# Kernel tuning notes

Hardware: AMD Instinct MI355X
Metric: run time of the kernel (lower is better)

## Reference

```python
import jax, jax.numpy as jnp
import numpy as np

N = 100000   # total nodes
E = 500000   # directed edges
G = 100      # graphs in batch (1000 nodes each)
D = 146      # in/hidden/out dim
C = 10       # classes
BN_EPS = 1e-5


def setup_inputs():
    key = jax.random.key(0)
    ks = jax.random.split(key, 20)
    nodes_feat = jax.random.normal(ks[0], (N, D), jnp.float32)
    src = jax.random.randint(ks[1], (E,), 0, N, dtype=jnp.int32)
    dst = jax.random.randint(ks[2], (E,), 0, N, dtype=jnp.int32)
    graph_ids = (jnp.arange(N, dtype=jnp.int32) // (N // G)).astype(jnp.int32)
    snorm = jnp.full((N,), 1.0 / np.sqrt(N // G), jnp.float32)
    s = 0.05
    W_emb = jax.random.normal(ks[3], (D, D), jnp.float32) * s
    b_emb = jnp.zeros((D,), jnp.float32)
    Ws = jax.random.normal(ks[4], (4, D, D), jnp.float32) * s
    bs = jnp.zeros((4, D), jnp.float32)
    gammas = jnp.ones((4, D), jnp.float32)
    betas = jnp.zeros((4, D), jnp.float32)
    W1 = jax.random.normal(ks[5], (D, D // 2), jnp.float32) * s
    b1 = jnp.zeros((D // 2,), jnp.float32)
    W2 = jax.random.normal(ks[6], (D // 2, D // 4), jnp.float32) * s
    b2 = jnp.zeros((D // 4,), jnp.float32)
    W3 = jax.random.normal(ks[7], (D // 4, C), jnp.float32) * s
    b3 = jnp.zeros((C,), jnp.float32)
    return dict(nodes_feat=nodes_feat, snorm=snorm, W_emb=W_emb, b_emb=b_emb,
                Ws=Ws, bs=bs, gammas=gammas, betas=betas,
                W1=W1, b1=b1, W2=W2, b2=b2, W3=W3, b3=b3,
                src=src, dst=dst, graph_ids=graph_ids)


def _gcn_layer(h, W, b, gamma, beta, src, dst, norm_out, norm_in, snorm):
    h_in = h
    # GraphConv norm='both': D_out^{-1/2} on source, sum-aggregate, D_in^{-1/2} on dest
    m = (h * norm_out[:, None])[src]                     # [E, D] gather
    agg = jax.ops.segment_sum(m, dst, num_segments=N)    # [N, D] scatter-add
    h = agg * norm_in[:, None] @ W + b                   # linear
    h = h * snorm[:, None]                               # graph norm
    mu = jnp.mean(h, axis=0)
    var = jnp.var(h, axis=0)
    h = (h - mu) * jax.lax.rsqrt(var + BN_EPS) * gamma + beta  # batch norm
    h = jax.nn.relu(h)
    return h_in + h                                      # residual


def reference(nodes_feat, snorm, W_emb, b_emb, Ws, bs, gammas, betas,
              W1, b1, W2, b2, W3, b3, src, dst, graph_ids):
    ones_e = jnp.ones((E,), jnp.float32)
    deg_out = jnp.clip(jax.ops.segment_sum(ones_e, src, num_segments=N), 1.0)
    deg_in = jnp.clip(jax.ops.segment_sum(ones_e, dst, num_segments=N), 1.0)
    norm_out = jax.lax.rsqrt(deg_out)
    norm_in = jax.lax.rsqrt(deg_in)

    h = nodes_feat @ W_emb + b_emb                       # embedding_h
    for i in range(4):
        h = _gcn_layer(h, Ws[i], bs[i], gammas[i], betas[i],
                       src, dst, norm_out, norm_in, snorm)

    # mean_nodes per graph
    cnt = jax.ops.segment_sum(jnp.ones((N,), jnp.float32), graph_ids, num_segments=G)
    hg = jax.ops.segment_sum(h, graph_ids, num_segments=G) / cnt[:, None]

    # MLPReadout: 146 -> 73 -> 36 -> 10
    x = jax.nn.relu(hg @ W1 + b1)
    x = jax.nn.relu(x @ W2 + b2)
    return x @ W3 + b3
```

## Files before the change

kernel.cpp:

```cpp
#include <hip/hip_runtime.h>

#define N_NODES 100000
#define N_EDGES 500000
#define N_GRAPHS 100
#define DIM 146
#define APAD 160
#define HPAD 160
#define TPW 160
#define BN_EPS 1e-5f
#define GS_PART 8
#define GS_STRIDE 147
#define ST_PART 4

typedef __bf16 bf16x8 __attribute__((ext_vector_type(8)));
typedef float floatx4 __attribute__((ext_vector_type(4)));
typedef unsigned short ushort_t;
typedef unsigned int uint_t;

__device__ inline ushort_t f2bf(float x) {
  uint_t u = __float_as_uint(x);
  uint_t r = (u + 0x7fffu + ((u >> 16) & 1u)) >> 16;
  return (ushort_t)r;
}
__device__ inline float bf2f(ushort_t b) { return __uint_as_float((uint_t)b << 16); }
__device__ inline uint_t pack2bf(float a, float b) {
  return (uint_t)f2bf(a) | ((uint_t)f2bf(b) << 16);
}
__device__ inline float bflo(uint_t u) { return __uint_as_float(u << 16); }
__device__ inline float bfhi(uint_t u) { return __uint_as_float(u & 0xffff0000u); }

__device__ inline void async_cp16(const ushort_t* g, ushort_t* l) {
  __builtin_amdgcn_global_load_lds((const __attribute__((address_space(1))) void*)g,
                                   (__attribute__((address_space(3))) void*)l, 16, 0, 0);
}

__global__ void hist_kernel(const int* __restrict__ src, const int* __restrict__ dst,
                            int* __restrict__ deg_out, int* __restrict__ deg_in) {
  int e = blockIdx.x * 256 + threadIdx.x;
  if (e < N_EDGES) {
    atomicAdd(&deg_out[src[e]], 1);
    atomicAdd(&deg_in[dst[e]], 1);
  }
}

__global__ void norm_kernel(const int* __restrict__ deg_out, const int* __restrict__ deg_in,
                            float* __restrict__ norm_out, float* __restrict__ norm_in) {
  int v = blockIdx.x * 256 + threadIdx.x;
  if (v < N_NODES) {
    norm_out[v] = rsqrtf((float)max(deg_out[v], 1));
    norm_in[v]  = rsqrtf((float)max(deg_in[v], 1));
  }
}

__global__ void scan1_kernel(const int* __restrict__ deg_in, int* __restrict__ bsums) {
  __shared__ int sred[256];
  int t0 = blockIdx.x * 1024 + threadIdx.x * 4;
  int s = 0;
#pragma unroll
  for (int i = 0; i < 4; i++) { int v = t0 + i; s += (v < N_NODES) ? deg_in[v] : 0; }
  sred[threadIdx.x] = s; __syncthreads();
  for (int off = 128; off > 0; off >>= 1) {
    if (threadIdx.x < off) sred[threadIdx.x] += sred[threadIdx.x + off];
    __syncthreads();
  }
  if (threadIdx.x == 0) bsums[blockIdx.x] = sred[0];
}

__global__ void scan2_kernel(const int* __restrict__ bsums, int* __restrict__ bofs,
                             int* __restrict__ row_ptr, int nb) {
  if (threadIdx.x == 0 && blockIdx.x == 0) {
    int run = 0;
    for (int i = 0; i < nb; i++) { bofs[i] = run; run += bsums[i]; }
    row_ptr[N_NODES] = run;
  }
}

__global__ void scan3_kernel(const int* __restrict__ deg_in, const int* __restrict__ bofs,
                             int* __restrict__ row_ptr) {
  __shared__ int ssc[256];
  int t0 = blockIdx.x * 1024 + threadIdx.x * 4;
  int v4[4]; int s = 0;
#pragma unroll
  for (int i = 0; i < 4; i++) { int v = t0 + i; v4[i] = (v < N_NODES) ? deg_in[v] : 0; s += v4[i]; }
  ssc[threadIdx.x] = s; __syncthreads();
  for (int off = 1; off < 256; off <<= 1) {
    int t = (threadIdx.x >= off) ? ssc[threadIdx.x - off] : 0;
    __syncthreads();
    ssc[threadIdx.x] += t;
    __syncthreads();
  }
  int ex = ssc[threadIdx.x] - s + bofs[blockIdx.x];
#pragma unroll
  for (int i = 0; i < 4; i++) {
    int v = t0 + i;
    if (v < N_NODES) { row_ptr[v] = ex; ex += v4[i]; }
  }
}

__global__ void csr_fill_kernel(const int* __restrict__ src, const int* __restrict__ dst,
                                const int* __restrict__ row_ptr, int* __restrict__ fill,
                                int* __restrict__ csr) {
  int e = blockIdx.x * 256 + threadIdx.x;
  if (e < N_EDGES) {
    int d = dst[e];
    int slot = atomicAdd(&fill[d], 1);
    csr[row_ptr[d] + slot] = src[e];
  }
}

__global__ void wtrans_kernel(const float* __restrict__ W_emb, const float* __restrict__ Ws,
                              ushort_t* __restrict__ Wb, ushort_t* __restrict__ Wh) {
  int idx = blockIdx.x * 256 + threadIdx.x;
  if (idx >= 5 * 5 * 10 * 64 * 8) return;
  int j = idx & 7;
  int t = idx >> 3;
  int lane = t & 63; t >>= 6;
  int nt = t % 10; t /= 10;
  int kc = t % 5;
  int m = t / 5;
  const float* W = (m == 0) ? W_emb : Ws + (size_t)(m - 1) * DIM * DIM;
  int k = kc * 32 + (lane >> 4) * 8 + j;
  int n = nt * 16 + (lane & 15);
  float w = (k < DIM && n < DIM) ? W[k * DIM + n] : 0.f;
  ushort_t hi = f2bf(w);
  float lo = w - bf2f(hi);
  size_t base = (size_t)((((m * 5 + kc) * 10 + nt) * 2) * 64 + lane) * 8 + j;
  Wb[base] = hi;
  Wb[base + 512] = f2bf(lo);
  Wh[(size_t)(((m * 5 + kc) * 10 + nt) * 64 + lane) * 8 + j] = hi;
}

__device__ inline bf16x8 make_frag(const float* __restrict__ nf, int row, int kc, int quad) {
  union { bf16x8 v; ushort_t u[8]; } r;
  const float* p = nf + (size_t)row * DIM + kc * 32 + quad * 8;
  int c0 = kc * 32 + quad * 8;
  if (c0 + 8 <= DIM) {
    float2 q0 = *(const float2*)(p);
    float2 q1 = *(const float2*)(p + 2);
    float2 q2 = *(const float2*)(p + 4);
    float2 q3 = *(const float2*)(p + 6);
    r.u[0] = f2bf(q0.x); r.u[1] = f2bf(q0.y); r.u[2] = f2bf(q1.x); r.u[3] = f2bf(q1.y);
    r.u[4] = f2bf(q2.x); r.u[5] = f2bf(q2.y); r.u[6] = f2bf(q3.x); r.u[7] = f2bf(q3.y);
  } else {
#pragma unroll
    for (int j = 0; j < 8; j++) r.u[j] = (c0 + j < DIM) ? f2bf(p[j]) : (ushort_t)0;
  }
  return r.v;
}

__global__ __launch_bounds__(256, 3) void gemm_embed_kernel(
    const float* __restrict__ nf, const ushort_t* __restrict__ Wb,
    const float* __restrict__ bias, const float* __restrict__ norm_out,
    float* __restrict__ h, ushort_t* __restrict__ hb) {
  __shared__ __align__(16) ushort_t sB[2][10240];
  int wave = threadIdx.x >> 6, lane = threadIdx.x & 63;
  int quad = lane >> 4, l16 = lane & 15;
  int m0 = blockIdx.x * 128 + wave * 32;
  int ra = min(m0 + l16, N_NODES - 1);
  int rb = min(m0 + 16 + l16, N_NODES - 1);

  auto stage = [&](int buf, int kc) {
    const ushort_t* wsrc = Wb + (size_t)kc * 10240 + threadIdx.x * 8;
    ushort_t* ldst = &sB[buf][threadIdx.x * 8];
#pragma unroll
    for (int p = 0; p < 5; p++) async_cp16(wsrc + p * 2048, ldst + p * 2048);
  };

  stage(0, 0);
  __syncthreads();

  floatx4 acc[2][10];
#pragma unroll
  for (int s = 0; s < 2; s++)
#pragma unroll
    for (int nt = 0; nt < 10; nt++) acc[s][nt] = (floatx4){0.f, 0.f, 0.f, 0.f};

#pragma unroll
  for (int kc = 0; kc < 5; kc++) {
    int buf = kc & 1;
    if (kc < 4) stage(buf ^ 1, kc + 1);
    bf16x8 a0 = make_frag(nf, ra, kc, quad);
    bf16x8 a1 = make_frag(nf, rb, kc, quad);
    const ushort_t* bp = &sB[buf][lane * 8];
#pragma unroll
    for (int nt = 0; nt < 10; nt++) {
      bf16x8 bh = *(const bf16x8*)(bp + (nt * 2) * 512);
      bf16x8 bl = *(const bf16x8*)(bp + (nt * 2 + 1) * 512);
      acc[0][nt] = __builtin_amdgcn_mfma_f32_16x16x32_bf16(a0, bh, acc[0][nt], 0, 0, 0);
      acc[1][nt] = __builtin_amdgcn_mfma_f32_16x16x32_bf16(a1, bh, acc[1][nt], 0, 0, 0);
      acc[0][nt] = __builtin_amdgcn_mfma_f32_16x16x32_bf16(a0, bl, acc[0][nt], 0, 0, 0);
      acc[1][nt] = __builtin_amdgcn_mfma_f32_16x16x32_bf16(a1, bl, acc[1][nt], 0, 0, 0);
    }
    __syncthreads();
  }

  float no[2][4];
#pragma unroll
  for (int s = 0; s < 2; s++)
#pragma unroll
    for (int r = 0; r < 4; r++) no[s][r] = norm_out[min(m0 + s * 16 + quad * 4 + r, N_NODES - 1)];

  float* sF = (float*)&sB[0][0];
#pragma unroll
  for (int nt = 0; nt < 5; nt++) {
    int c = nt * 16 + l16;
    float b = bias[c];
#pragma unroll
    for (int s = 0; s < 2; s++)
#pragma unroll
      for (int r = 0; r < 4; r++)
        sF[(wave * 32 + s * 16 + quad * 4 + r) * 80 + c] = acc[s][nt][r] + b;
  }
  __syncthreads();
#pragma unroll
  for (int i = 0; i < 10; i++) {
    int n = threadIdx.x + i * 256;
    int row = n / 20, ch = n - row * 20;
    int grow = blockIdx.x * 128 + row;
    if (grow < N_NODES)
      *((uint4*)(h + (size_t)grow * HPAD) + ch) = ((const uint4*)(sF + row * 80))[ch];
  }
  __syncthreads();
#pragma unroll
  for (int nt = 5; nt < 10; nt++) {
    int c = nt * 16 + l16;
    float b = (c < DIM) ? bias[c] : 0.f;
#pragma unroll
    for (int s = 0; s < 2; s++)
#pragma unroll
      for (int r = 0; r < 4; r++)
        sF[(wave * 32 + s * 16 + quad * 4 + r) * 80 + (c - 80)] = acc[s][nt][r] + b;
  }
  __syncthreads();
#pragma unroll
  for (int i = 0; i < 10; i++) {
    int n = threadIdx.x + i * 256;
    int row = n / 20, ch = n - row * 20;
    int grow = blockIdx.x * 128 + row;
    if (grow < N_NODES)
      *((uint4*)(h + (size_t)grow * HPAD + 80) + ch) = ((const uint4*)(sF + row * 80))[ch];
  }
  __syncthreads();
  ushort_t* sC = &sB[0][0];
#pragma unroll
  for (int nt = 0; nt < 10; nt++) {
    int c = nt * 16 + l16;
    float b = (c < DIM) ? bias[c] : 0.f;
#pragma unroll
    for (int s = 0; s < 2; s++)
#pragma unroll
      for (int r = 0; r < 4; r++)
        sC[(wave * 32 + s * 16 + quad * 4 + r) * 160 + c] = f2bf((acc[s][nt][r] + b) * no[s][r]);
  }
  __syncthreads();
#pragma unroll
  for (int i = 0; i < 10; i++) {
    int n = threadIdx.x + i * 256;
    int row = n / 20, ch = n - row * 20;
    int grow = blockIdx.x * 128 + row;
    if (grow < N_NODES)
      *((uint4*)(hb + (size_t)grow * APAD) + ch) = ((const uint4*)(sC + row * 160))[ch];
  }
}

__global__ __launch_bounds__(256, 4) void gemm_kernel(
    const ushort_t* __restrict__ Abf, const ushort_t* __restrict__ Wh,
    const float* __restrict__ bias, const float* __restrict__ snorm,
    ushort_t* __restrict__ tmpb, float* __restrict__ stats) {
  __shared__ __align__(16) ushort_t sB[2][5120];
  __shared__ float sred[2 * DIM];
  int wave = threadIdx.x >> 6, lane = threadIdx.x & 63;
  int quad = lane >> 4, l16 = lane & 15;
  int m0 = blockIdx.x * 128 + wave * 32;
  int ra = min(m0 + l16, N_NODES - 1);
  int rb = min(m0 + 16 + l16, N_NODES - 1);
  const ushort_t* ap0 = Abf + (size_t)ra * APAD + quad * 8;
  const ushort_t* ap1 = Abf + (size_t)rb * APAD + quad * 8;

  auto stage = [&](int buf, int kc) {
    const ushort_t* wsrc = Wh + (size_t)kc * 5120;
    ushort_t* ldst = &sB[buf][0];
    async_cp16(wsrc + threadIdx.x * 8, ldst + threadIdx.x * 8);
    async_cp16(wsrc + (threadIdx.x + 256) * 8, ldst + (threadIdx.x + 256) * 8);
    if (threadIdx.x < 128)
      async_cp16(wsrc + (threadIdx.x + 512) * 8, ldst + (threadIdx.x + 512) * 8);
  };

  stage(0, 0);
  bf16x8 a0[5], a1[5];
#pragma unroll
  for (int kc = 0; kc < 5; kc++) {
    a0[kc] = *(const bf16x8*)(ap0 + kc * 32);
    a1[kc] = *(const bf16x8*)(ap1 + kc * 32);
  }
  for (int i = threadIdx.x; i < 2 * DIM; i += 256) sred[i] = 0.f;
  __syncthreads();

  floatx4 acc[2][10];
#pragma unroll
  for (int s = 0; s < 2; s++)
#pragma unroll
    for (int nt = 0; nt < 10; nt++) acc[s][nt] = (floatx4){0.f, 0.f, 0.f, 0.f};

  for (int kc = 0; kc < 5; kc++) {
    int buf = kc & 1;
    if (kc < 4) stage(buf ^ 1, kc + 1);
    const ushort_t* bp = &sB[buf][lane * 8];
#pragma unroll
    for (int nt = 0; nt < 10; nt++) {
      bf16x8 bh = *(const bf16x8*)(bp + nt * 512);
      acc[0][nt] = __builtin_amdgcn_mfma_f32_16x16x32_bf16(a0[kc], bh, acc[0][nt], 0, 0, 0);
      acc[1][nt] = __builtin_amdgcn_mfma_f32_16x16x32_bf16(a1[kc], bh, acc[1][nt], 0, 0, 0);
    }
    __syncthreads();
  }

  float sn[2][4];
#pragma unroll
  for (int s = 0; s < 2; s++)
#pragma unroll
    for (int r = 0; r < 4; r++) sn[s][r] = snorm[min(m0 + s * 16 + quad * 4 + r, N_NODES - 1)];
#pragma unroll
  for (int nt = 0; nt < 10; nt++) {
    int c = nt * 16 + l16;
    if (c < DIM) {
      float b = bias[c];
      float ssum = 0.f, ssq = 0.f;
#pragma unroll
      for (int s = 0; s < 2; s++)
#pragma unroll
        for (int r = 0; r < 4; r++) {
          if (m0 + s * 16 + quad * 4 + r < N_NODES) {
            float val = (acc[s][nt][r] + b) * sn[s][r];
            ssum += val; ssq += val * val;
          }
        }
      ssum += __shfl_xor(ssum, 16, 64); ssum += __shfl_xor(ssum, 32, 64);
      ssq  += __shfl_xor(ssq, 16, 64);  ssq  += __shfl_xor(ssq, 32, 64);
      if (quad == 0) {
        atomicAdd(&sred[c], ssum);
        atomicAdd(&sred[DIM + c], ssq);
      }
    }
  }

  ushort_t* sC = &sB[0][0];
#pragma unroll
  for (int half = 0; half < 2; half++) {
    __syncthreads();
    if ((wave >> 1) == half) {
      int lrow = (wave & 1) * 32;
#pragma unroll
      for (int nt = 0; nt < 10; nt++) {
        int c = nt * 16 + l16;
        float b = (c < DIM) ? bias[c] : 0.f;
#pragma unroll
        for (int s = 0; s < 2; s++)
#pragma unroll
          for (int r = 0; r < 4; r++)
            sC[(lrow + s * 16 + quad * 4 + r) * TPW + c] = f2bf((acc[s][nt][r] + b) * sn[s][r]);
      }
    }
    __syncthreads();
    uint4* gp = (uint4*)(tmpb + ((size_t)blockIdx.x * 128 + half * 64) * TPW);
#pragma unroll
    for (int i = 0; i < 5; i++) {
      int n = threadIdx.x + i * 256;
      gp[n] = *(const uint4*)(sC + n * 8);
    }
  }
  float* stp = stats + (blockIdx.x & (ST_PART - 1)) * 2 * DIM;
  for (int i = threadIdx.x; i < 2 * DIM; i += 256) atomicAdd(&stp[i], sred[i]);
}

__global__ __launch_bounds__(256) void agg_kernel(
    const ushort_t* __restrict__ hb, const int* __restrict__ row_ptr,
    const int* __restrict__ csr, const float* __restrict__ norm_in,
    ushort_t* __restrict__ xb) {
  int wid = threadIdx.x >> 6, lane = threadIdx.x & 63;
  int v = blockIdx.x * 4 + wid;
  if (v >= N_NODES) return;
  int e0 = row_ptr[v], e1 = row_ptr[v + 1];
  bool act = lane < 40;
  int col8 = lane * 4;
  float a0 = 0.f, a1 = 0.f, a2 = 0.f, a3 = 0.f;
  float b0 = 0.f, b1 = 0.f, b2 = 0.f, b3 = 0.f;
  float c0 = 0.f, c1 = 0.f, c2 = 0.f, c3 = 0.f;
  float d0 = 0.f, d1 = 0.f, d2 = 0.f, d3 = 0.f;
  int e = e0;
  for (; e + 3 < e1; e += 4) {
    int s0 = csr[e], s1 = csr[e + 1], s2 = csr[e + 2], s3 = csr[e + 3];
    if (act) {
      uint2 u0 = *(const uint2*)(hb + (size_t)s0 * APAD + col8);
      uint2 u1 = *(const uint2*)(hb + (size_t)s1 * APAD + col8);
      uint2 u2 = *(const uint2*)(hb + (size_t)s2 * APAD + col8);
      uint2 u3 = *(const uint2*)(hb + (size_t)s3 * APAD + col8);
      a0 += bflo(u0.x); a1 += bfhi(u0.x); a2 += bflo(u0.y); a3 += bfhi(u0.y);
      b0 += bflo(u1.x); b1 += bfhi(u1.x); b2 += bflo(u1.y); b3 += bfhi(u1.y);
      c0 += bflo(u2.x); c1 += bfhi(u2.x); c2 += bflo(u2.y); c3 += bfhi(u2.y);
      d0 += bflo(u3.x); d1 += bfhi(u3.x); d2 += bflo(u3.y); d3 += bfhi(u3.y);
    }
  }
  for (; e < e1; e++) {
    int s0 = csr[e];
    if (act) {
      uint2 u0 = *(const uint2*)(hb + (size_t)s0 * APAD + col8);
      a0 += bflo(u0.x); a1 += bfhi(u0.x); a2 += bflo(u0.y); a3 += bfhi(u0.y);
    }
  }
  if (act) {
    float ni = norm_in[v];
    uint2 o;
    o.x = pack2bf((a0 + b0 + c0 + d0) * ni, (a1 + b1 + c1 + d1) * ni);
    o.y = pack2bf((a2 + b2 + c2 + d2) * ni, (a3 + b3 + c3 + d3) * ni);
    *(uint2*)((uint_t*)(xb + (size_t)v * APAD) + lane * 2) = o;
  }
}

__global__ __launch_bounds__(256) void bn_kernel(const ushort_t* __restrict__ tmpb,
                                                 const float* __restrict__ stats,
                                                 const float* __restrict__ gamma,
                                                 const float* __restrict__ beta,
                                                 const float* __restrict__ norm_out,
                                                 float* __restrict__ h,
                                                 ushort_t* __restrict__ hb) {
  __shared__ float2 scs[DIM / 2], shs[DIM / 2];
  int t = threadIdx.x;
  if (t < DIM / 2) {
    int c0 = 2 * t, c1 = c0 + 1;
    float su0 = 0.f, su1 = 0.f, sq0 = 0.f, sq1 = 0.f;
#pragma unroll
    for (int p = 0; p < ST_PART; p++) {
      const float* sp = stats + p * 2 * DIM;
      su0 += sp[c0]; su1 += sp[c1];
      sq0 += sp[DIM + c0]; sq1 += sp[DIM + c1];
    }
    float mu0 = su0 * (1.f / N_NODES), mu1 = su1 * (1.f / N_NODES);
    float v0 = sq0 * (1.f / N_NODES) - mu0 * mu0;
    float v1 = sq1 * (1.f / N_NODES) - mu1 * mu1;
    float s0 = gamma[c0] * rsqrtf(v0 + BN_EPS), s1 = gamma[c1] * rsqrtf(v1 + BN_EPS);
    scs[t] = make_float2(s0, s1);
    shs[t] = make_float2(beta[c0] - mu0 * s0, beta[c1] - mu1 * s1);
  }
  __syncthreads();
  int idx = blockIdx.x * 256 + t;
  if (idx >= N_NODES * (DIM / 2)) return;
  int v = idx / (DIM / 2), c2 = idx - v * (DIM / 2);
  uint_t tu = ((const uint_t*)tmpb)[(size_t)v * (TPW / 2) + c2];
  float2 sc = scs[c2], sh = shs[c2];
  float2* hp = (float2*)(h + (size_t)v * HPAD + 2 * c2);
  float2 hv = *hp;
  float x0 = fmaf(bflo(tu), sc.x, sh.x); x0 = fmaxf(x0, 0.f);
  float x1 = fmaf(bfhi(tu), sc.y, sh.y); x1 = fmaxf(x1, 0.f);
  hv.x += x0; hv.y += x1;
  *hp = hv;
  float no = norm_out[v];
  ((uint_t*)hb)[(size_t)v * (APAD / 2) + c2] = pack2bf(hv.x * no, hv.y * no);
}

__global__ __launch_bounds__(192) void gsum_kernel(
    const ushort_t* __restrict__ tmpb, const float* __restrict__ stats,
    const float* __restrict__ gamma, const float* __restrict__ beta,
    const float* __restrict__ h, const int* __restrict__ gids,
    float* __restrict__ hgp) {
  int t = threadIdx.x;
  if (t > DIM) return;
  float sc = 0.f, sh = 0.f;
  if (t < DIM) {
    float su = 0.f, sq = 0.f;
#pragma unroll
    for (int p = 0; p < ST_PART; p++) {
      const float* sp = stats + p * 2 * DIM;
      su += sp[t]; sq += sp[DIM + t];
    }
    float mu = su * (1.f / N_NODES);
    float var = sq * (1.f / N_NODES) - mu * mu;
    sc = gamma[t] * rsqrtf(var + BN_EPS);
    sh = beta[t] - mu * sc;
  }
  int r0 = blockIdx.x * 64;
  int part = blockIdx.x & (GS_PART - 1);
  float accv = 0.f;
  int g_prev = gids[r0];
  for (int rr = 0; rr < 64; rr++) {
    int r = r0 + rr;
    if (r >= N_NODES) break;
    int g = gids[r];
    if (g != g_prev) {
      atomicAdd(&hgp[(size_t)(part * N_GRAPHS + g_prev) * GS_STRIDE + t], accv);
      accv = 0.f; g_prev = g;
    }
    float val;
    if (t < DIM) {
      float x = fmaf(bf2f(tmpb[(size_t)r * TPW + t]), sc, sh);
      x = fmaxf(x, 0.f);
      val = h[(size_t)r * HPAD + t] + x;
    } else {
      val = 1.f;
    }
    accv += val;
  }
  atomicAdd(&hgp[(size_t)(part * N_GRAPHS + g_prev) * GS_STRIDE + t], accv);
}

__global__ __launch_bounds__(256) void mlp_kernel(
    const float* __restrict__ hgp,
    const float* __restrict__ W1, const float* __restrict__ b1,
    const float* __restrict__ W2, const float* __restrict__ b2,
    const float* __restrict__ W3, const float* __restrict__ b3,
    float* __restrict__ out) {
  __shared__ float hrow[DIM];
  __shared__ float x1[73];
  __shared__ float x2[36];
  int g = blockIdx.x;
  int t = threadIdx.x;
  if (t < DIM) {
    float s = 0.f, cnt = 0.f;
#pragma unroll
    for (int p = 0; p < GS_PART; p++) {
      const float* row = hgp + (size_t)(p * N_GRAPHS + g) * GS_STRIDE;
      s += row[t];
      cnt += row[DIM];
    }
    hrow[t] = s / cnt;
  }
  __syncthreads();
  if (t < 73) {
    float s = b1[t];
    for (int k = 0; k < DIM; k++) s = fmaf(hrow[k], W1[k * 73 + t], s);
    x1[t] = s > 0.f ? s : 0.f;
  }
  __syncthreads();
  if (t < 36) {
    float s = b2[t];
    for (int k = 0; k < 73; k++) s = fmaf(x1[k], W2[k * 36 + t], s);
    x2[t] = s > 0.f ? s : 0.f;
  }
  __syncthreads();
  if (t < 10) {
    float s = b3[t];
    for (int k = 0; k < 36; k++) s = fmaf(x2[k], W3[k * 10 + t], s);
    out[g * 10 + t] = s;
  }
}

extern "C" void kernel_launch(void* const* d_in, const int* in_sizes, int n_in,
                              void* d_out, int out_size, void* d_ws, size_t ws_size,
                              hipStream_t stream) {
  const float* nodes_feat = (const float*)d_in[0];
  const float* snorm  = (const float*)d_in[1];
  const float* W_emb  = (const float*)d_in[2];
  const float* b_emb  = (const float*)d_in[3];
  const float* Ws     = (const float*)d_in[4];
  const float* bs     = (const float*)d_in[5];
  const float* gammas = (const float*)d_in[6];
  const float* betas  = (const float*)d_in[7];
  const float* W1 = (const float*)d_in[8];
  const float* b1 = (const float*)d_in[9];
  const float* W2 = (const float*)d_in[10];
  const float* b2 = (const float*)d_in[11];
  const float* W3 = (const float*)d_in[12];
  const float* b3 = (const float*)d_in[13];
  const int* src  = (const int*)d_in[14];
  const int* dst  = (const int*)d_in[15];
  const int* gids = (const int*)d_in[16];
  float* out = (float*)d_out;

  const int GB = (N_NODES + 127) / 128;
  const int NPADROWS = GB * 128;

  char* base = (char*)d_ws;
  size_t off = 0;
  auto alloc = [&](size_t bytes) { void* p = base + off; off += (bytes + 255) & ~size_t(255); return p; };
  float* h    = (float*)alloc((size_t)N_NODES * HPAD * 4);
  ushort_t* tmpb = (ushort_t*)alloc((size_t)NPADROWS * TPW * 2);
  ushort_t* xb = (ushort_t*)alloc((size_t)N_NODES * APAD * 2);
  ushort_t* hb = (ushort_t*)alloc((size_t)N_NODES * APAD * 2);
  char* zstart = base + off;
  int* deg_out = (int*)alloc(N_NODES * 4);
  int* deg_in  = (int*)alloc(N_NODES * 4);
  int* fill    = (int*)alloc(N_NODES * 4);
  float* stats = (float*)alloc(4 * ST_PART * 2 * DIM * 4);
  float* hgp   = (float*)alloc((size_t)GS_PART * N_GRAPHS * GS_STRIDE * 4);
  size_t zbytes = (size_t)((base + off) - zstart);
  int* row_ptr = (int*)alloc((N_NODES + 1) * 4);
  float* norm_out = (float*)alloc(N_NODES * 4);
  float* norm_in  = (float*)alloc(N_NODES * 4);
  int* csr   = (int*)alloc((size_t)N_EDGES * 4);
  int* bsums = (int*)alloc(128 * 4);
  int* bofs  = (int*)alloc(128 * 4);
  ushort_t* Wb = (ushort_t*)alloc((size_t)5 * 5 * 10 * 2 * 64 * 8 * 2);
  ushort_t* Wh = (ushort_t*)alloc((size_t)5 * 5 * 10 * 64 * 8 * 2);

  hipMemsetAsync(zstart, 0, zbytes, stream);

  hist_kernel<<<(N_EDGES + 255) / 256, 256, 0, stream>>>(src, dst, deg_out, deg_in);
  norm_kernel<<<(N_NODES + 255) / 256, 256, 0, stream>>>(deg_out, deg_in, norm_out, norm_in);
  int nb = (N_NODES + 1023) / 1024;
  scan1_kernel<<<nb, 256, 0, stream>>>(deg_in, bsums);
  scan2_kernel<<<1, 64, 0, stream>>>(bsums, bofs, row_ptr, nb);
  scan3_kernel<<<nb, 256, 0, stream>>>(deg_in, bofs, row_ptr);
  csr_fill_kernel<<<(N_EDGES + 255) / 256, 256, 0, stream>>>(src, dst, row_ptr, fill, csr);
  wtrans_kernel<<<(5 * 5 * 10 * 64 * 8 + 255) / 256, 256, 0, stream>>>(W_emb, Ws, Wb, Wh);

  const size_t WHM = (size_t)5 * 10 * 64 * 8;

  gemm_embed_kernel<<<GB, 256, 0, stream>>>(nodes_feat, Wb, b_emb, norm_out, h, hb);

  for (int l = 0; l < 4; l++) {
    float* st = stats + (size_t)l * ST_PART * 2 * DIM;
    agg_kernel<<<(N_NODES + 3) / 4, 256, 0, stream>>>(hb, row_ptr, csr, norm_in, xb);
    gemm_kernel<<<GB, 256, 0, stream>>>(xb, Wh + (size_t)(l + 1) * WHM, bs + l * DIM,
                                        snorm, tmpb, st);
    if (l < 3) {
      bn_kernel<<<(N_NODES * (DIM / 2) + 255) / 256, 256, 0, stream>>>(
          tmpb, st, gammas + l * DIM, betas + l * DIM, norm_out, h, hb);
    } else {
      gsum_kernel<<<(N_NODES + 63) / 64, 192, 0, stream>>>(
          tmpb, st, gammas + l * DIM, betas + l * DIM, h, gids, hgp);
    }
  }

  mlp_kernel<<<N_GRAPHS, 256, 0, stream>>>(hgp, W1, b1, W2, b2, W3, b3, out);
}
```

Before: 708.4 us.

## Keep residual hidden state only in bf16 and apply norm_out during aggregation

Removes the fp32 hidden-state buffer and the separate pre-scaled bf16 copy, keeping a single unscaled bf16 hidden state. The residual add in bn and gsum now reads and writes this bf16 buffer, and the source degree normalisation moves into the gather-sum as an fma. The embedding GEMM drops the hi/lo split-bf16 weights and the fp32 output pass, halving its MFMA and weight staging work. This cuts memory traffic per layer but accumulates bf16 rounding in the residual path across four layers, which may raise error against the reference.

```diff
diff --git a/kernel.cpp b/kernel.cpp
--- a/kernel.cpp
+++ b/kernel.cpp
@@ -5,7 +5,6 @@
 #define N_GRAPHS 100
 #define DIM 146
 #define APAD 160
-#define HPAD 160
 #define TPW 160
 #define BN_EPS 1e-5f
 #define GS_PART 8
@@ -109,7 +108,7 @@
 }
 
 __global__ void wtrans_kernel(const float* __restrict__ W_emb, const float* __restrict__ Ws,
-                              ushort_t* __restrict__ Wb, ushort_t* __restrict__ Wh) {
+                              ushort_t* __restrict__ Wh) {
   int idx = blockIdx.x * 256 + threadIdx.x;
   if (idx >= 5 * 5 * 10 * 64 * 8) return;
   int j = idx & 7;
@@ -122,12 +121,7 @@
   int k = kc * 32 + (lane >> 4) * 8 + j;
   int n = nt * 16 + (lane & 15);
   float w = (k < DIM && n < DIM) ? W[k * DIM + n] : 0.f;
-  ushort_t hi = f2bf(w);
-  float lo = w - bf2f(hi);
-  size_t base = (size_t)((((m * 5 + kc) * 10 + nt) * 2) * 64 + lane) * 8 + j;
-  Wb[base] = hi;
-  Wb[base + 512] = f2bf(lo);
-  Wh[(size_t)(((m * 5 + kc) * 10 + nt) * 64 + lane) * 8 + j] = hi;
+  Wh[(size_t)(((m * 5 + kc) * 10 + nt) * 64 + lane) * 8 + j] = f2bf(w);
 }
 
 __device__ inline bf16x8 make_frag(const float* __restrict__ nf, int row, int kc, int quad) {
@@ -148,11 +142,10 @@
   return r.v;
 }
 
-__global__ __launch_bounds__(256, 3) void gemm_embed_kernel(
-    const float* __restrict__ nf, const ushort_t* __restrict__ Wb,
-    const float* __restrict__ bias, const float* __restrict__ norm_out,
-    float* __restrict__ h, ushort_t* __restrict__ hb) {
-  __shared__ __align__(16) ushort_t sB[2][10240];
+__global__ __launch_bounds__(256, 4) void gemm_embed_kernel(
+    const float* __restrict__ nf, const ushort_t* __restrict__ Wh,
+    const float* __restrict__ bias, ushort_t* __restrict__ hbf) {
+  __shared__ __align__(16) ushort_t sB[2][5120];
   int wave = threadIdx.x >> 6, lane = threadIdx.x & 63;
   int quad = lane >> 4, l16 = lane & 15;
   int m0 = blockIdx.x * 128 + wave * 32;
@@ -160,10 +153,12 @@
   int rb = min(m0 + 16 + l16, N_NODES - 1);
 
   auto stage = [&](int buf, int kc) {
-    const ushort_t* wsrc = Wb + (size_t)kc * 10240 + threadIdx.x * 8;
-    ushort_t* ldst = &sB[buf][threadIdx.x * 8];
-#pragma unroll
-    for (int p = 0; p < 5; p++) async_cp16(wsrc + p * 2048, ldst + p * 2048);
+    const ushort_t* wsrc = Wh + (size_t)kc * 5120;
+    ushort_t* ldst = &sB[buf][0];
+    async_cp16(wsrc + threadIdx.x * 8, ldst + threadIdx.x * 8);
+    async_cp16(wsrc + (threadIdx.x + 256) * 8, ldst + (threadIdx.x + 256) * 8);
+    if (threadIdx.x < 128)
+      async_cp16(wsrc + (threadIdx.x + 512) * 8, ldst + (threadIdx.x + 512) * 8);
   };
 
   stage(0, 0);
@@ -175,7 +170,6 @@
 #pragma unroll
     for (int nt = 0; nt < 10; nt++) acc[s][nt] = (floatx4){0.f, 0.f, 0.f, 0.f};
 
-#pragma unroll
   for (int kc = 0; kc < 5; kc++) {
     int buf = kc & 1;
     if (kc < 4) stage(buf ^ 1, kc + 1);
@@ -184,82 +178,37 @@
     const ushort_t* bp = &sB[buf][lane * 8];
 #pragma unroll
     for (int nt = 0; nt < 10; nt++) {
-      bf16x8 bh = *(const bf16x8*)(bp + (nt * 2) * 512);
-      bf16x8 bl = *(const bf16x8*)(bp + (nt * 2 + 1) * 512);
+      bf16x8 bh = *(const bf16x8*)(bp + nt * 512);
       acc[0][nt] = __builtin_amdgcn_mfma_f32_16x16x32_bf16(a0, bh, acc[0][nt], 0, 0, 0);
       acc[1][nt] = __builtin_amdgcn_mfma_f32_16x16x32_bf16(a1, bh, acc[1][nt], 0, 0, 0);
-      acc[0][nt] = __builtin_amdgcn_mfma_f32_16x16x32_bf16(a0, bl, acc[0][nt], 0, 0, 0);
-      acc[1][nt] = __builtin_amdgcn_mfma_f32_16x16x32_bf16(a1, bl, acc[1][nt], 0, 0, 0);
-    }
-    __syncthreads();
-  }
-
-  float no[2][4];
-#pragma unroll
-  for (int s = 0; s < 2; s++)
-#pragma unroll
-    for (int r = 0; r < 4; r++) no[s][r] = norm_out[min(m0 + s * 16 + quad * 4 + r, N_NODES - 1)];
-
-  float* sF = (float*)&sB[0][0];
-#pragma unroll
-  for (int nt = 0; nt < 5; nt++) {
-    int c = nt * 16 + l16;
-    float b = bias[c];
-#pragma unroll
-    for (int s = 0; s < 2; s++)
-#pragma unroll
-      for (int r = 0; r < 4; r++)
-        sF[(wave * 32 + s * 16 + quad * 4 + r) * 80 + c] = acc[s][nt][r] + b;
-  }
-  __syncthreads();
-#pragma unroll
-  for (int i = 0; i < 10; i++) {
-    int n = threadIdx.x + i * 256;
-    int row = n / 20, ch = n - row * 20;
-    int grow = blockIdx.x * 128 + row;
-    if (grow < N_NODES)
-      *((uint4*)(h + (size_t)grow * HPAD) + ch) = ((const uint4*)(sF + row * 80))[ch];
-  }
-  __syncthreads();
-#pragma unroll
-  for (int nt = 5; nt < 10; nt++) {
-    int c = nt * 16 + l16;
-    float b = (c < DIM) ? bias[c] : 0.f;
-#pragma unroll
-    for (int s = 0; s < 2; s++)
-#pragma unroll
-      for (int r = 0; r < 4; r++)
-        sF[(wave * 32 + s * 16 + quad * 4 + r) * 80 + (c - 80)] = acc[s][nt][r] + b;
-  }
-  __syncthreads();
-#pragma unroll
-  for (int i = 0; i < 10; i++) {
-    int n = threadIdx.x + i * 256;
-    int row = n / 20, ch = n - row * 20;
-    int grow = blockIdx.x * 128 + row;
-    if (grow < N_NODES)
-      *((uint4*)(h + (size_t)grow * HPAD + 80) + ch) = ((const uint4*)(sF + row * 80))[ch];
-  }
-  __syncthreads();
+    }
+    __syncthreads();
+  }
+
   ushort_t* sC = &sB[0][0];
 #pragma unroll
-  for (int nt = 0; nt < 10; nt++) {
-    int c = nt * 16 + l16;
-    float b = (c < DIM) ? bias[c] : 0.f;
-#pragma unroll
-    for (int s = 0; s < 2; s++)
-#pragma unroll
-      for (int r = 0; r < 4; r++)
-        sC[(wave * 32 + s * 16 + quad * 4 + r) * 160 + c] = f2bf((acc[s][nt][r] + b) * no[s][r]);
-  }
-  __syncthreads();
-#pragma unroll
-  for (int i = 0; i < 10; i++) {
-    int n = threadIdx.x + i * 256;
-    int row = n / 20, ch = n - row * 20;
-    int grow = blockIdx.x * 128 + row;
-    if (grow < N_NODES)
-      *((uint4*)(hb + (size_t)grow * APAD) + ch) = ((const uint4*)(sC + row * 160))[ch];
+  for (int half = 0; half < 2; half++) {
+    __syncthreads();
+    if ((wave >> 1) == half) {
+      int lrow = (wave & 1) * 32;
+#pragma unroll
+      for (int nt = 0; nt < 10; nt++) {
+        int c = nt * 16 + l16;
+        float b = (c < DIM) ? bias[c] : 0.f;
+#pragma unroll
+        for (int s = 0; s < 2; s++)
+#pragma unroll
+          for (int r = 0; r < 4; r++)
+            sC[(lrow + s * 16 + quad * 4 + r) * 160 + c] = f2bf(acc[s][nt][r] + b);
+      }
+    }
+    __syncthreads();
+    uint4* gp = (uint4*)(hbf + ((size_t)blockIdx.x * 128 + half * 64) * APAD);
+#pragma unroll
+    for (int i = 0; i < 5; i++) {
+      int n = threadIdx.x + i * 256;
+      gp[n] = *(const uint4*)(sC + n * 8);
+    }
   }
 }
 
@@ -374,9 +323,9 @@
 }
 
 __global__ __launch_bounds__(256) void agg_kernel(
-    const ushort_t* __restrict__ hb, const int* __restrict__ row_ptr,
-    const int* __restrict__ csr, const float* __restrict__ norm_in,
-    ushort_t* __restrict__ xb) {
+    const ushort_t* __restrict__ hbf, const int* __restrict__ row_ptr,
+    const int* __restrict__ csr, const float* __restrict__ norm_out,
+    const float* __restrict__ norm_in, ushort_t* __restrict__ xb) {
   int wid = threadIdx.x >> 6, lane = threadIdx.x & 63;
   int v = blockIdx.x * 4 + wid;
   if (v >= N_NODES) return;
@@ -390,22 +339,29 @@
   int e = e0;
   for (; e + 3 < e1; e += 4) {
     int s0 = csr[e], s1 = csr[e + 1], s2 = csr[e + 2], s3 = csr[e + 3];
+    float n0 = norm_out[s0], n1 = norm_out[s1], n2 = norm_out[s2], n3 = norm_out[s3];
     if (act) {
-      uint2 u0 = *(const uint2*)(hb + (size_t)s0 * APAD + col8);
-      uint2 u1 = *(const uint2*)(hb + (size_t)s1 * APAD + col8);
-      uint2 u2 = *(const uint2*)(hb + (size_t)s2 * APAD + col8);
-      uint2 u3 = *(const uint2*)(hb + (size_t)s3 * APAD + col8);
-      a0 += bflo(u0.x); a1 += bfhi(u0.x); a2 += bflo(u0.y); a3 += bfhi(u0.y);
-      b0 += bflo(u1.x); b1 += bfhi(u1.x); b2 += bflo(u1.y); b3 += bfhi(u1.y);
-      c0 += bflo(u2.x); c1 += bfhi(u2.x); c2 += bflo(u2.y); c3 += bfhi(u2.y);
-      d0 += bflo(u3.x); d1 += bfhi(u3.x); d2 += bflo(u3.y); d3 += bfhi(u3.y);
+      uint2 u0 = *(const uint2*)(hbf + (size_t)s0 * APAD + col8);
+      uint2 u1 = *(const uint2*)(hbf + (size_t)s1 * APAD + col8);
+      uint2 u2 = *(const uint2*)(hbf + (size_t)s2 * APAD + col8);
+      uint2 u3 = *(const uint2*)(hbf + (size_t)s3 * APAD + col8);
+      a0 = fmaf(bflo(u0.x), n0, a0); a1 = fmaf(bfhi(u0.x), n0, a1);
+      a2 = fmaf(bflo(u0.y), n0, a2); a3 = fmaf(bfhi(u0.y), n0, a3);
+      b0 = fmaf(bflo(u1.x), n1, b0); b1 = fmaf(bfhi(u1.x), n1, b1);
+      b2 = fmaf(bflo(u1.y), n1, b2); b3 = fmaf(bfhi(u1.y), n1, b3);
+      c0 = fmaf(bflo(u2.x), n2, c0); c1 = fmaf(bfhi(u2.x), n2, c1);
+      c2 = fmaf(bflo(u2.y), n2, c2); c3 = fmaf(bfhi(u2.y), n2, c3);
+      d0 = fmaf(bflo(u3.x), n3, d0); d1 = fmaf(bfhi(u3.x), n3, d1);
+      d2 = fmaf(bflo(u3.y), n3, d2); d3 = fmaf(bfhi(u3.y), n3, d3);
     }
   }
   for (; e < e1; e++) {
     int s0 = csr[e];
+    float n0 = norm_out[s0];
     if (act) {
-      uint2 u0 = *(const uint2*)(hb + (size_t)s0 * APAD + col8);
-      a0 += bflo(u0.x); a1 += bfhi(u0.x); a2 += bflo(u0.y); a3 += bfhi(u0.y);
+      uint2 u0 = *(const uint2*)(hbf + (size_t)s0 * APAD + col8);
+      a0 = fmaf(bflo(u0.x), n0, a0); a1 = fmaf(bfhi(u0.x), n0, a1);
+      a2 = fmaf(bflo(u0.y), n0, a2); a3 = fmaf(bfhi(u0.y), n0, a3);
     }
   }
   if (act) {
@@ -421,9 +377,7 @@
                                                  const float* __restrict__ stats,
                                                  const float* __restrict__ gamma,
                                                  const float* __restrict__ beta,
-                                                 const float* __restrict__ norm_out,
-                                                 float* __restrict__ h,
-                                                 ushort_t* __restrict__ hb) {
+                                                 ushort_t* __restrict__ hbf) {
   __shared__ float2 scs[DIM / 2], shs[DIM / 2];
   int t = threadIdx.x;
   if (t < DIM / 2) {
@@ -447,21 +401,17 @@
   if (idx >= N_NODES * (DIM / 2)) return;
   int v = idx / (DIM / 2), c2 = idx - v * (DIM / 2);
   uint_t tu = ((const uint_t*)tmpb)[(size_t)v * (TPW / 2) + c2];
+  uint_t hu = ((const uint_t*)hbf)[(size_t)v * (APAD / 2) + c2];
   float2 sc = scs[c2], sh = shs[c2];
-  float2* hp = (float2*)(h + (size_t)v * HPAD + 2 * c2);
-  float2 hv = *hp;
   float x0 = fmaf(bflo(tu), sc.x, sh.x); x0 = fmaxf(x0, 0.f);
   float x1 = fmaf(bfhi(tu), sc.y, sh.y); x1 = fmaxf(x1, 0.f);
-  hv.x += x0; hv.y += x1;
-  *hp = hv;
-  float no = norm_out[v];
-  ((uint_t*)hb)[(size_t)v * (APAD / 2) + c2] = pack2bf(hv.x * no, hv.y * no);
+  ((uint_t*)hbf)[(size_t)v * (APAD / 2) + c2] = pack2bf(bflo(hu) + x0, bfhi(hu) + x1);
 }
 
 __global__ __launch_bounds__(192) void gsum_kernel(
     const ushort_t* __restrict__ tmpb, const float* __restrict__ stats,
     const float* __restrict__ gamma, const float* __restrict__ beta,
-    const float* __restrict__ h, const int* __restrict__ gids,
+    const ushort_t* __restrict__ hbf, const int* __restrict__ gids,
     float* __restrict__ hgp) {
   int t = threadIdx.x;
   if (t > DIM) return;
@@ -494,7 +444,7 @@
     if (t < DIM) {
       float x = fmaf(bf2f(tmpb[(size_t)r * TPW + t]), sc, sh);
       x = fmaxf(x, 0.f);
-      val = h[(size_t)r * HPAD + t] + x;
+      val = bf2f(hbf[(size_t)r * APAD + t]) + x;
     } else {
       val = 1.f;
     }
@@ -572,10 +522,9 @@
   char* base = (char*)d_ws;
   size_t off = 0;
   auto alloc = [&](size_t bytes) { void* p = base + off; off += (bytes + 255) & ~size_t(255); return p; };
-  float* h    = (float*)alloc((size_t)N_NODES * HPAD * 4);
+  ushort_t* hbf  = (ushort_t*)alloc((size_t)NPADROWS * APAD * 2);
   ushort_t* tmpb = (ushort_t*)alloc((size_t)NPADROWS * TPW * 2);
-  ushort_t* xb = (ushort_t*)alloc((size_t)N_NODES * APAD * 2);
-  ushort_t* hb = (ushort_t*)alloc((size_t)N_NODES * APAD * 2);
+  ushort_t* xb   = (ushort_t*)alloc((size_t)N_NODES * APAD * 2);
   char* zstart = base + off;
   int* deg_out = (int*)alloc(N_NODES * 4);
   int* deg_in  = (int*)alloc(N_NODES * 4);
@@ -589,7 +538,6 @@
   int* csr   = (int*)alloc((size_t)N_EDGES * 4);
   int* bsums = (int*)alloc(128 * 4);
   int* bofs  = (int*)alloc(128 * 4);
-  ushort_t* Wb = (ushort_t*)alloc((size_t)5 * 5 * 10 * 2 * 64 * 8 * 2);
   ushort_t* Wh = (ushort_t*)alloc((size_t)5 * 5 * 10 * 64 * 8 * 2);
 
   hipMemsetAsync(zstart, 0, zbytes, stream);
@@ -601,23 +549,23 @@
   scan2_kernel<<<1, 64, 0, stream>>>(bsums, bofs, row_ptr, nb);
   scan3_kernel<<<nb, 256, 0, stream>>>(deg_in, bofs, row_ptr);
   csr_fill_kernel<<<(N_EDGES + 255) / 256, 256, 0, stream>>>(src, dst, row_ptr, fill, csr);
-  wtrans_kernel<<<(5 * 5 * 10 * 64 * 8 + 255) / 256, 256, 0, stream>>>(W_emb, Ws, Wb, Wh);
+  wtrans_kernel<<<(5 * 5 * 10 * 64 * 8 + 255) / 256, 256, 0, stream>>>(W_emb, Ws, Wh);
 
   const size_t WHM = (size_t)5 * 10 * 64 * 8;
 
-  gemm_embed_kernel<<<GB, 256, 0, stream>>>(nodes_feat, Wb, b_emb, norm_out, h, hb);
+  gemm_embed_kernel<<<GB, 256, 0, stream>>>(nodes_feat, Wh, b_emb, hbf);
 
   for (int l = 0; l < 4; l++) {
     float* st = stats + (size_t)l * ST_PART * 2 * DIM;
-    agg_kernel<<<(N_NODES + 3) / 4, 256, 0, stream>>>(hb, row_ptr, csr, norm_in, xb);
+    agg_kernel<<<(N_NODES + 3) / 4, 256, 0, stream>>>(hbf, row_ptr, csr, norm_out, norm_in, xb);
     gemm_kernel<<<GB, 256, 0, stream>>>(xb, Wh + (size_t)(l + 1) * WHM, bs + l * DIM,
                                         snorm, tmpb, st);
     if (l < 3) {
       bn_kernel<<<(N_NODES * (DIM / 2) + 255) / 256, 256, 0, stream>>>(
-          tmpb, st, gammas + l * DIM, betas + l * DIM, norm_out, h, hb);
+          tmpb, st, gammas + l * DIM, betas + l * DIM, hbf);
     } else {
       gsum_kernel<<<(N_NODES + 63) / 64, 192, 0, stream>>>(
-          tmpb, st, gammas + l * DIM, betas + l * DIM, h, gids, hgp);
+          tmpb, st, gammas + l * DIM, betas + l * DIM, hbf, gids, hgp);
     }
   }
 
```

Measured after the change: 679.5 us. -4.1%, faster.
